# Optimization experiments

Measured on AMD Instinct MI355X. Metric: run time of the kernel, lower is better.

Reference implementation:

```python
import jax, jax.numpy as jnp
import numpy as np
from jax import lax

# dims
B, T_MEL, N_MEL, L_TXT, D_TXT = 8, 400, 80, 128, 512
E, HID, EMB, N_SPK = 256, 256, 128, 100
H = HID // 2  # per-direction LSTM hidden


def setup_inputs() -> dict:
    key = jax.random.key(0)
    ks = jax.random.split(key, 16)
    def n(k, shape, s=0.02):
        return jax.random.normal(k, shape, jnp.float32) * s
    return {
        "x": n(ks[0], (B, N_MEL, T_MEL), 1.0),
        "input_lengths": jax.random.randint(ks[1], (B,), T_MEL // 2, T_MEL + 1).astype(jnp.int32),
        "text": n(ks[2], (B, L_TXT, D_TXT), 1.0),
        "text_lengths": jax.random.randint(ks[3], (B,), L_TXT // 2, L_TXT + 1).astype(jnp.int32),
        "Wx": n(ks[4], (E, N_MEL)), "bx": jnp.zeros((E,), jnp.float32),
        "Wq": n(ks[5], (E, D_TXT)), "bq": jnp.zeros((E,), jnp.float32),
        "Wout": n(ks[6], (E, E)), "bout": jnp.zeros((E,), jnp.float32),
        "v": jax.random.normal(ks[7], (E, 1), jnp.float32) * 0.1,
        "lstm_wih": n(ks[8], (2, 2, 4 * H, HID)),
        "lstm_whh": n(ks[9], (2, 2, 4 * H, H)),
        "lstm_bih": jnp.zeros((2, 2, 4 * H), jnp.float32),
        "lstm_bhh": jnp.zeros((2, 2, 4 * H), jnp.float32),
        "p1_w": n(ks[10], (EMB, HID)), "p1_b": jnp.zeros((EMB,), jnp.float32),
        "p2_w": n(ks[11], (N_SPK, EMB)), "p2_b": jnp.zeros((N_SPK,), jnp.float32),
    }


def _run_lstm(x, Wih, Whh, bih, bhh):
    # x: [B, L, in] -> outputs [B, L, H]; PyTorch gate order i,f,g,o
    h0 = jnp.zeros((x.shape[0], Whh.shape[1]), x.dtype)
    c0 = jnp.zeros_like(h0)
    def step(carry, xt):
        h, c = carry
        g = xt @ Wih.T + h @ Whh.T + (bih + bhh)
        i, f, gg, o = jnp.split(g, 4, axis=-1)
        c = jax.nn.sigmoid(f) * c + jax.nn.sigmoid(i) * jnp.tanh(gg)
        h = jax.nn.sigmoid(o) * jnp.tanh(c)
        return (h, c), h
    _, hs = lax.scan(step, (h0, c0), x.swapaxes(0, 1))  # scan over time
    return hs.swapaxes(0, 1)


def _reverse_by_length(x, lengths):
    # reverse the first lengths[b] steps of each sequence (pack_padded semantics)
    L = x.shape[1]
    idx = jnp.clip(lengths[:, None] - 1 - jnp.arange(L)[None, :], 0, L - 1)
    return jnp.take_along_axis(x, idx[:, :, None], axis=1)


def reference(x, input_lengths, text, text_lengths, Wx, bx, Wq, bq, Wout, bout, v,
              lstm_wih, lstm_whh, lstm_bih, lstm_bhh, p1_w, p1_b, p2_w, p2_b):
    # ---- vectorized VanillaAttention over all text tokens ----
    mels = x.swapaxes(1, 2)                       # [B, T, M]
    x1 = mels @ Wx.T + bx                         # [B, T, E]   linear_x
    q1 = text @ Wq.T + bq                         # [B, L, E]   linear_q
    # v^T @ out_linear(tanh(.)) == tanh(.) @ (Wout^T v) + v . bout
    w = Wout.T @ v[:, 0]                          # [E]
    c = bout @ v[:, 0]                            # scalar
    s = jnp.tanh(x1[:, None, :, :] + q1[:, :, None, :])   # [B, L, T, E]
    scores = jnp.einsum('blte,e->blt', s, w) + c           # [B, L, T]
    mel_mask = jnp.arange(T_MEL)[None, :] < input_lengths[:, None]   # [B, T]
    scores = jnp.where(mel_mask[:, None, :], scores, -jnp.inf)
    scores = jax.nn.softmax(scores, axis=-1)
    contexts = jnp.einsum('blt,bte->ble', scores, x1)       # [B, L, E]
    h = q1 + contexts                                       # LSTM input

    # ---- 2-layer bidirectional LSTM (packed semantics via per-length reversal) ----
    for layer in range(2):
        fwd = _run_lstm(h, lstm_wih[layer, 0], lstm_whh[layer, 0], lstm_bih[layer, 0], lstm_bhh[layer, 0])
        rev = _reverse_by_length(h, text_lengths)
        bwd = _run_lstm(rev, lstm_wih[layer, 1], lstm_whh[layer, 1], lstm_bih[layer, 1], lstm_bhh[layer, 1])
        bwd = _reverse_by_length(bwd, text_lengths)
        h = jnp.concatenate([fwd, bwd], axis=-1)            # [B, L, HID]

    # ---- masked mean pool (pad_packed zeros the padding before the sum) ----
    txt_mask = (jnp.arange(L_TXT)[None, :] < text_lengths[:, None]).astype(h.dtype)
    pooled = (h * txt_mask[:, :, None]).sum(axis=1) / text_lengths[:, None].astype(h.dtype)

    out = jnp.tanh(pooled @ p1_w.T + p1_b)
    embeddings = out / jnp.linalg.norm(out, axis=1, keepdims=True)
    logits = out @ p2_w.T + p2_b
    return logits, embeddings, scores
```

## Files before the change

### kernel.cpp

```cpp
#include <hip/hip_runtime.h>
#include <hip/hip_bf16.h>
#include <math.h>

#define B 8
#define T_MEL 400
#define N_MEL 80
#define L_TXT 128
#define D_TXT 512
#define E 256
#define HID 256
#define EMB 128
#define N_SPK 100
#define HH 128

#define OFF_W      0
#define OFF_C      256
#define OFF_WXT    272
#define OFF_WQT    (OFF_WXT + N_MEL*E)
#define OFF_WIHT   (OFF_WQT + D_TXT*E)
#define OFF_BSUM   (OFF_WIHT + 2*2*256*512)
#define OFF_X1     (OFF_BSUM + 2048)
#define OFF_Q1     (OFF_X1 + B*T_MEL*E)
#define OFF_G      OFF_X1
#define OFF_H0     (OFF_Q1 + B*L_TXT*E)
#define OFF_O1     (OFF_H0 + B*L_TXT*E)
#define OFF_HS0    OFF_H0
#define OFF_POOL   OFF_O1
#define OFF_WG     (OFF_O1 + 4096)

typedef _Float16 half2v __attribute__((ext_vector_type(2)));

__device__ __forceinline__ float fast_sigmoid(float x){ return 1.f/(1.f+__expf(-x)); }
__device__ __forceinline__ float fast_tanh(float x){ float e=__expf(2.f*x); return 1.f - 2.f/(e+1.f); }

__device__ __forceinline__ float fdot2(uint a, uint b, float c){
  half2v ha = __builtin_bit_cast(half2v, a);
  half2v hb = __builtin_bit_cast(half2v, b);
#if __has_builtin(__builtin_amdgcn_fdot2)
  return __builtin_amdgcn_fdot2(ha, hb, c, false);
#else
  float r;
  asm("v_dot2_f32_f16 %0, %1, %2, %3" : "=v"(r) : "v"(a), "v"(b), "v"(c));
  return r;
#endif
}
__device__ __forceinline__ uint packh2(float a, float b){
  union { _Float16 h[2]; uint u; } x;
  x.h[0] = (_Float16)a; x.h[1] = (_Float16)b; return x.u;
}

__global__ __launch_bounds__(256) void k_prep(const float* __restrict__ Wout, const float* __restrict__ bout,
                       const float* __restrict__ v,    const float* __restrict__ Wx,
                       const float* __restrict__ Wq,   const float* __restrict__ wih,
                       const float* __restrict__ bih,  const float* __restrict__ bhh,
                       const float* __restrict__ whh,  float* __restrict__ ws){
  __shared__ __align__(16) float tile[64][81];
  __shared__ __align__(16) uint  utile[64][129];
  int blk = blockIdx.x, tid = threadIdx.x;
  if (blk == 0){
    float acc = 0.f;
    for (int j=0;j<E;j++) acc += Wout[j*E + tid] * v[j];
    ws[OFF_W + tid] = acc;
    if (tid==0){ float c=0.f; for(int j=0;j<E;j++) c += bout[j]*v[j]; ws[OFF_C]=c; }
  } else if (blk <= 4){
    int e0 = (blk-1)*64;
    for (int idx = tid; idx < 64*20; idx += 256){
      int e = idx/20, c4 = idx%20;
      float4 vv = *(const float4*)&Wx[(size_t)(e0+e)*N_MEL + 4*c4];
      tile[e][4*c4]=vv.x; tile[e][4*c4+1]=vv.y; tile[e][4*c4+2]=vv.z; tile[e][4*c4+3]=vv.w;
    }
    __syncthreads();
    for (int idx = tid; idx < N_MEL*64; idx += 256){
      int m = idx>>6, e = idx&63;
      ws[OFF_WXT + m*E + e0 + e] = tile[e][m];
    }
  } else if (blk <= 36){
    int t = blk-5; int e0 = (t&3)*64, k0 = (t>>2)*64;
    for (int idx = tid; idx < 64*16; idx += 256){
      int e = idx>>4, c = idx&15;
      float4 vv = *(const float4*)&Wq[(size_t)(e0+e)*D_TXT + k0 + 4*c];
      tile[e][4*c]=vv.x; tile[e][4*c+1]=vv.y; tile[e][4*c+2]=vv.z; tile[e][4*c+3]=vv.w;
    }
    __syncthreads();
    for (int idx = tid; idx < 64*64; idx += 256){
      int k = idx>>6, e = idx&63;
      ws[OFF_WQT + (k0+k)*E + e0 + e] = tile[e][k];
    }
  } else if (blk <= 68){
    int t = blk-37; int ld = t>>3, g0 = (t&7)*64;
    for (int idx = tid; idx < 64*64; idx += 256){
      int g = idx>>6, c = idx&63;
      float4 vv = *(const float4*)&wih[((size_t)(ld*512+g0+g))*256 + 4*c];
      utile[g][2*c]   = packh2(vv.x, vv.y);
      utile[g][2*c+1] = packh2(vv.z, vv.w);
    }
    __syncthreads();
    uint* wout = (uint*)(ws + OFF_WIHT) + (size_t)ld*128*512;
    for (int idx = tid; idx < 128*64; idx += 256){
      int k2 = idx>>6, g = idx&63;
      wout[(size_t)k2*512 + g0 + g] = utile[g][k2];
    }
  } else if (blk == 69){
    for (int i = tid; i < 2048; i += 256)
      ws[OFF_BSUM + i] = bih[i] + bhh[i];
  } else {
    int bp = blk - 70;
    int ld = bp >> 2, w = bp & 3;
    uint* wg = (uint*)(ws + OFF_WG) + ((size_t)ld*4 + w)*8192;
    for (int ii = 0; ii < 32; ii++){
      int i = ii*256 + tid;
      int r  = i >> 11;
      int jj = (i >> 8) & 7;
      int l  = (i >> 2) & 63;
      int k  = i & 3;
      int u  = w*32 + (l >> 1);
      int hf = l & 1;
      const float* src = whh + ((size_t)(ld*512 + r*128 + u))*HH + 64*hf + jj*8 + 2*k;
      wg[i] = packh2(src[0], src[1]);
    }
  }
}

__global__ __launch_bounds__(256) void k_xq(const float* __restrict__ x,    const float* __restrict__ bx,
                                            const float* __restrict__ text, const float* __restrict__ bq,
                                            float* __restrict__ ws){
  __shared__ float sbuf[2048];
  int blk = blockIdx.x, tid = threadIdx.x;
  if (blk < 800){
    int b = blk/100; int t0 = (blk%100)*4;
    float (*sx)[4] = (float(*)[4])sbuf;
    for (int i = tid; i < N_MEL*4; i += 256){
      int m = i>>2, ii = i&3;
      sx[m][ii] = x[(b*N_MEL+m)*T_MEL + t0 + ii];
    }
    __syncthreads();
    float bxe = bx[tid];
    float a0=bxe,a1=bxe,a2=bxe,a3=bxe;
    const float* wxt = ws + OFF_WXT;
    #pragma unroll 4
    for (int m=0;m<N_MEL;m++){
      float w = wxt[m*E + tid];
      a0 += sx[m][0]*w; a1 += sx[m][1]*w; a2 += sx[m][2]*w; a3 += sx[m][3]*w;
    }
    float* x1 = ws + OFF_X1 + (b*T_MEL + t0)*E + tid;
    x1[0]=a0; x1[E]=a1; x1[2*E]=a2; x1[3*E]=a3;
  } else {
    int bb = blk - 800;
    int b = bb/32; int l0 = (bb%32)*4;
    float (*st)[D_TXT] = (float(*)[D_TXT])sbuf;
    for (int i = tid; i < 4*D_TXT; i += 256){
      int li = i / D_TXT, k = i % D_TXT;
      st[li][k] = text[(b*L_TXT + l0 + li)*D_TXT + k];
    }
    __syncthreads();
    float bqe = bq[tid];
    float a0=bqe,a1=bqe,a2=bqe,a3=bqe;
    const float* wqt = ws + OFF_WQT;
    #pragma unroll 2
    for (int k=0;k<D_TXT;k++){
      float w = wqt[k*E + tid];
      a0 += st[0][k]*w; a1 += st[1][k]*w; a2 += st[2][k]*w; a3 += st[3][k]*w;
    }
    float* q1 = ws + OFF_Q1 + (b*L_TXT + l0)*E + tid;
    q1[0]=a0; q1[E]=a1; q1[2*E]=a2; q1[3*E]=a3;
  }
}

__global__ __launch_bounds__(256) void k_score(const int* __restrict__ mel_len,
                                               float* __restrict__ ws,
                                               float* __restrict__ d_out){
  int blk = blockIdx.x; int b = blk >> 7; int l = blk & 127;
  int tid = threadIdx.x; int lane = tid & 63; int wv = tid >> 6;
  __shared__ __align__(16) float sl[T_MEL];
  __shared__ float red[8];
  const float* x1 = ws + OFF_X1 + b*T_MEL*E;
  const float* q1 = ws + OFF_Q1 + (b*L_TXT+l)*E;
  int g = lane >> 4, i = lane & 15;
  float qv[16], wvv[16];
  {
    const float4* q4 = (const float4*)(q1 + i*16);
    const float4* w4 = (const float4*)(ws + OFF_W + i*16);
    #pragma unroll
    for (int j=0;j<4;j++){
      float4 a = q4[j]; qv[4*j]=a.x; qv[4*j+1]=a.y; qv[4*j+2]=a.z; qv[4*j+3]=a.w;
      float4 c = w4[j]; wvv[4*j]=c.x; wvv[4*j+1]=c.y; wvv[4*j+2]=c.z; wvv[4*j+3]=c.w;
    }
  }
  float cc = ws[OFF_C];
  int len = mel_len[b];
  #pragma unroll 2
  for (int iter=0; iter<25; iter++){
    int t = iter*16 + wv*4 + g;
    const float4* xr = (const float4*)(x1 + t*E + i*16);
    float s = 0.f;
    #pragma unroll
    for (int j=0;j<4;j++){
      float4 xv = xr[j];
      s += wvv[4*j+0]*fast_tanh(xv.x + qv[4*j+0]);
      s += wvv[4*j+1]*fast_tanh(xv.y + qv[4*j+1]);
      s += wvv[4*j+2]*fast_tanh(xv.z + qv[4*j+2]);
      s += wvv[4*j+3]*fast_tanh(xv.w + qv[4*j+3]);
    }
    s += __shfl_xor(s,1); s += __shfl_xor(s,2);
    s += __shfl_xor(s,4); s += __shfl_xor(s,8);
    if (i==0) sl[t] = s + cc;
  }
  __syncthreads();
  float mx = -3.0e38f;
  for (int t = tid; t < T_MEL; t += 256) if (t < len) mx = fmaxf(mx, sl[t]);
  #pragma unroll
  for (int off=32; off>=1; off>>=1) mx = fmaxf(mx, __shfl_xor(mx, off));
  if (lane==0) red[wv] = mx;
  __syncthreads();
  mx = fmaxf(fmaxf(red[0],red[1]),fmaxf(red[2],red[3]));
  float se = 0.f;
  for (int t = tid; t < T_MEL; t += 256){
    float p = (t < len) ? __expf(sl[t]-mx) : 0.f;
    sl[t] = p; se += p;
  }
  #pragma unroll
  for (int off=32; off>=1; off>>=1) se += __shfl_xor(se, off);
  if (lane==0) red[4+wv] = se;
  __syncthreads();
  float rsum = 1.f/(red[4]+red[5]+red[6]+red[7]);
  float* sc_out = d_out + 1824 + (b*L_TXT + l)*T_MEL;
  for (int t = tid; t < T_MEL; t += 256){
    float p = sl[t]*rsum;
    sl[t] = p; sc_out[t] = p;
  }
  __syncthreads();
  float a = 0.f;
  int e = tid;
  for (int t = 0; t < T_MEL; t += 4){
    float4 p4 = *(const float4*)&sl[t];
    a += p4.x*x1[(t  )*E+e] + p4.y*x1[(t+1)*E+e]
       + p4.z*x1[(t+2)*E+e] + p4.w*x1[(t+3)*E+e];
  }
  ws[OFF_H0 + (b*L_TXT+l)*E + e] = q1[e] + a;
}

__global__ __launch_bounds__(512) void k_gates(const float* __restrict__ in,
                                               const float* __restrict__ hs,
                                               const int* __restrict__ txt_len,
                                               float* __restrict__ gates, int layer,
                                               float* __restrict__ ws){
  int idx = blockIdx.x; int tt = idx & 15; int dir = (idx>>4)&1; int b = idx>>5;
  int tid = threadIdx.x;
  __shared__ __align__(16) uint sih[8][128];
  __shared__ float outb[8][512];
  int len = txt_len[b];
  for (int i = tid; i < 8*128; i += 512){
    int r = i >> 7, k2 = i & 127;
    int t = tt*8 + r;
    int row = dir ? max(0, len-1-t) : t;
    float va, vb;
    if (layer == 0){
      const float2 p = *(const float2*)&in[((size_t)(b*L_TXT + row))*HID + 2*k2];
      va = p.x; vb = p.y;
    } else {
      int k = 2*k2; int d = k >> 7, u = k & 127;
      int sidx = (d==0) ? row : (row < len ? len-1-row : 0);
      const float2 p = *(const float2*)&hs[(((size_t)d*L_TXT + sidx)*8 + b)*128 + u];
      va = p.x; vb = p.y;
    }
    sih[r][k2] = packh2(va, vb);
  }
  __syncthreads();
  int ld = layer*2 + dir;
  int g = tid;
  float bsum = ws[OFF_BSUM + ld*512 + g];
  float acc[8];
  #pragma unroll
  for (int r=0;r<8;r++) acc[r] = bsum;
  const uint* wt2 = (const uint*)(ws + OFF_WIHT) + (size_t)ld*128*512 + g;
  for (int k4=0; k4<128; k4+=4){
    uint w0 = wt2[(k4  )*512];
    uint w1 = wt2[(k4+1)*512];
    uint w2 = wt2[(k4+2)*512];
    uint w3 = wt2[(k4+3)*512];
    #pragma unroll
    for (int r=0;r<8;r++){
      uint4 s4 = *(const uint4*)&sih[r][k4];
      acc[r] = fdot2(s4.x, w0, acc[r]);
      acc[r] = fdot2(s4.y, w1, acc[r]);
      acc[r] = fdot2(s4.z, w2, acc[r]);
      acc[r] = fdot2(s4.w, w3, acc[r]);
    }
  }
  #pragma unroll
  for (int r=0;r<8;r++) outb[r][g] = acc[r];
  __syncthreads();
  float* go = gates + (((size_t)(dir*L_TXT + tt*8)*8) + b)*512;
  int src = (tid & 3)*128 + (tid >> 2);
  #pragma unroll
  for (int r=0;r<8;r++) go[(size_t)r*8*512 + tid] = outb[r][src];
}

__global__ __launch_bounds__(256) void k_scan(const float* __restrict__ Gp,
                                              const uint* __restrict__ wg,
                                              const int* __restrict__ txt_len,
                                              float* __restrict__ hseq,
                                              float* __restrict__ pooled, int layer){
  __shared__ uint wlds[22528];
  int dir = blockIdx.x & 1; int b = blockIdx.x >> 1;
  int tid = threadIdx.x;
  int l = tid & 63, w = tid >> 6;
  int u  = tid >> 1;
  int hf = tid & 1;

  const uint* wgp = wg + (((size_t)(layer*2+dir))*4 + w)*8192 + l*4;
  uint4 wi[8], wf[8], wgg[8], wo[8];
  #pragma unroll
  for (int jj=0;jj<8;jj++){
    wi [jj] = *(const uint4*)(wgp + (jj   )*256);
    wf [jj] = *(const uint4*)(wgp + ( 8+jj)*256);
    wgg[jj] = *(const uint4*)(wgp + (16+jj)*256);
    wo [jj] = *(const uint4*)(wgp + (24+jj)*256);
  }
  #pragma unroll
  for (int jj=0;jj<8;jj++){
    asm volatile("" : "+v"(wi [jj].x), "+v"(wi [jj].y), "+v"(wi [jj].z), "+v"(wi [jj].w));
    asm volatile("" : "+v"(wf [jj].x), "+v"(wf [jj].y), "+v"(wf [jj].z), "+v"(wf [jj].w));
    asm volatile("" : "+v"(wgg[jj].x), "+v"(wgg[jj].y), "+v"(wgg[jj].z), "+v"(wgg[jj].w));
    asm volatile("" : "+v"(wo [jj].x), "+v"(wo [jj].y), "+v"(wo [jj].z), "+v"(wo [jj].w));
  }

  if (tid < 128) wlds[tid] = 0;
  int len = txt_len[b];
  bool pool = (layer == 1);

  const float* gb = Gp + ((size_t)(dir*L_TXT)*8 + b)*512 + u*4;
  float4 q = *(const float4*)gb;
  float c_reg = 0.f, psum = 0.f;
  __syncthreads();

  for (int s=0; s<L_TXT; s++){
    const float* gn = gb + (size_t)(s+1 < L_TXT ? s+1 : s)*4096;
    float4 qn = *(const float4*)gn;
    const uint4* hp = (const uint4*)(wlds + (s&1)*64 + hf*32);
    float a0 = hf ? 0.f : q.x;
    float a1 = hf ? 0.f : q.y;
    float a2 = hf ? 0.f : q.z;
    float a3 = hf ? 0.f : q.w;
    #pragma unroll
    for (int jj=0;jj<8;jj++){
      uint4 hv = hp[jj];
      uint4 w0 = wi [jj];
      uint4 w1 = wf [jj];
      uint4 w2 = wgg[jj];
      uint4 w3 = wo [jj];
      a0 = fdot2(w0.x,hv.x,a0); a0 = fdot2(w0.y,hv.y,a0);
      a0 = fdot2(w0.z,hv.z,a0); a0 = fdot2(w0.w,hv.w,a0);
      a1 = fdot2(w1.x,hv.x,a1); a1 = fdot2(w1.y,hv.y,a1);
      a1 = fdot2(w1.z,hv.z,a1); a1 = fdot2(w1.w,hv.w,a1);
      a2 = fdot2(w2.x,hv.x,a2); a2 = fdot2(w2.y,hv.y,a2);
      a2 = fdot2(w2.z,hv.z,a2); a2 = fdot2(w2.w,hv.w,a2);
      a3 = fdot2(w3.x,hv.x,a3); a3 = fdot2(w3.y,hv.y,a3);
      a3 = fdot2(w3.z,hv.z,a3); a3 = fdot2(w3.w,hv.w,a3);
    }
    a0 += __shfl_xor(a0, 1);
    a1 += __shfl_xor(a1, 1);
    a2 += __shfl_xor(a2, 1);
    a3 += __shfl_xor(a3, 1);
    float i_ = fast_sigmoid(a0);
    float f_ = fast_sigmoid(a1);
    float g_ = fast_tanh   (a2);
    float o_ = fast_sigmoid(a3);
    c_reg = f_*c_reg + i_*g_;
    float h = o_*fast_tanh(c_reg);
    float hn = __shfl_xor(h, 2);
    if (hf==0 && !(u&1)) wlds[((s+1)&1)*64 + (u>>1)] = packh2(h, hn);
    if (pool){
      if (s < len) psum += h;
    } else {
      if (hf==0) hseq[(((size_t)dir*L_TXT + s)*8 + b)*128 + u] = h;
    }
    q = qn;
    __syncthreads();
  }
  if (pool && hf==0) pooled[((size_t)(dir*8+b))*128 + u] = psum;
}

__global__ __launch_bounds__(256) void k_final(const float* __restrict__ pooled,
                                               const int* __restrict__ txt_len,
                                               const float* __restrict__ p1w,
                                               const float* __restrict__ p1b,
                                               const float* __restrict__ p2w,
                                               const float* __restrict__ p2b,
                                               float* __restrict__ d_out){
  int b = blockIdx.x; int tid = threadIdx.x;
  __shared__ float pl[HID];
  __shared__ float ol[EMB];
  __shared__ float nrm;
  int len = txt_len[b];
  int d = tid >> 7, u = tid & 127;
  pl[tid] = pooled[((size_t)(d*8+b))*128 + u] / (float)len;
  __syncthreads();
  if (tid < EMB){
    float a = p1b[tid];
    for (int k=0;k<HID;k++) a += pl[k]*p1w[tid*HID+k];
    ol[tid] = fast_tanh(a);
  }
  __syncthreads();
  if (tid == 0){
    float q = 0.f;
    for (int k=0;k<EMB;k++) q += ol[k]*ol[k];
    nrm = rsqrtf(q);
  }
  __syncthreads();
  if (tid < EMB) d_out[800 + b*EMB + tid] = ol[tid]*nrm;
  if (tid < N_SPK){
    float a = p2b[tid];
    for (int k=0;k<EMB;k++) a += ol[k]*p2w[tid*EMB+k];
    d_out[b*N_SPK + tid] = a;
  }
}

extern "C" void kernel_launch(void* const* d_in, const int* in_sizes, int n_in,
                              void* d_out, int out_size, void* d_ws, size_t ws_size,
                              hipStream_t stream) {
  const float* x       = (const float*)d_in[0];
  const int*   mel_len = (const int*)  d_in[1];
  const float* text    = (const float*)d_in[2];
  const int*   txt_len = (const int*)  d_in[3];
  const float* Wx      = (const float*)d_in[4];
  const float* bx      = (const float*)d_in[5];
  const float* Wq      = (const float*)d_in[6];
  const float* bq      = (const float*)d_in[7];
  const float* Wout    = (const float*)d_in[8];
  const float* bout    = (const float*)d_in[9];
  const float* v       = (const float*)d_in[10];
  const float* wih     = (const float*)d_in[11];
  const float* whh     = (const float*)d_in[12];
  const float* bih     = (const float*)d_in[13];
  const float* bhh     = (const float*)d_in[14];
  const float* p1w     = (const float*)d_in[15];
  const float* p1b     = (const float*)d_in[16];
  const float* p2w     = (const float*)d_in[17];
  const float* p2b     = (const float*)d_in[18];
  float* ws  = (float*)d_ws;
  float* out = (float*)d_out;
  const uint* wg = (const uint*)(ws + OFF_WG);

  k_prep <<<86, 256, 0, stream>>>(Wout, bout, v, Wx, Wq, wih, bih, bhh, whh, ws);
  k_xq   <<<1056, 256, 0, stream>>>(x, bx, text, bq, ws);
  k_score<<<1024, 256, 0, stream>>>(mel_len, ws, out);

  float* G = ws + OFF_G;
  k_gates<<<256, 512, 0, stream>>>(ws + OFF_H0, ws + OFF_HS0, txt_len, G, 0, ws);
  k_scan <<<16, 256, 0, stream>>>(G, wg, txt_len, ws + OFF_HS0, ws + OFF_POOL, 0);
  k_gates<<<256, 512, 0, stream>>>(ws + OFF_H0, ws + OFF_HS0, txt_len, G, 1, ws);
  k_scan <<<16, 256, 0, stream>>>(G, wg, txt_len, ws + OFF_HS0, ws + OFF_POOL, 1);

  k_final<<<8, 256, 0, stream>>>(ws + OFF_POOL, txt_len, p1w, p1b, p2w, p2b, out);
}
```

Measured before the change: 384.3 us.

## Split LSTM scan gates across twice as many threads per block

```diff
diff --git a/kernel.cpp b/kernel.cpp
--- a/kernel.cpp
+++ b/kernel.cpp
@@ -105,17 +105,19 @@
       ws[OFF_BSUM + i] = bih[i] + bhh[i];
   } else {
     int bp = blk - 70;
-    int ld = bp >> 2, w = bp & 3;
-    uint* wg = (uint*)(ws + OFF_WG) + ((size_t)ld*4 + w)*8192;
-    for (int ii = 0; ii < 32; ii++){
+    int ld = bp >> 3, w = bp & 7;
+    uint* wg = (uint*)(ws + OFF_WG) + ((size_t)ld*8 + w)*4096;
+    for (int ii = 0; ii < 16; ii++){
       int i = ii*256 + tid;
-      int r  = i >> 11;
-      int jj = (i >> 8) & 7;
+      int j  = i >> 8;
       int l  = (i >> 2) & 63;
       int k  = i & 3;
-      int u  = w*32 + (l >> 1);
+      int rsel = j >> 3, jj = j & 7;
+      int u  = w*16 + (l >> 2);
+      int pr = (l >> 1) & 1;
       int hf = l & 1;
-      const float* src = whh + ((size_t)(ld*512 + r*128 + u))*HH + 64*hf + jj*8 + 2*k;
+      int row = rsel ? (256 + pr*128 + u) : (pr*128 + u);
+      const float* src = whh + ((size_t)(ld*512 + row))*HH + 64*hf + jj*8 + 2*k;
       wg[i] = packh2(src[0], src[1]);
     }
   }
@@ -296,7 +298,7 @@
   for (int r=0;r<8;r++) go[(size_t)r*8*512 + tid] = outb[r][src];
 }
 
-__global__ __launch_bounds__(256) void k_scan(const float* __restrict__ Gp,
+__global__ __launch_bounds__(512) void k_scan(const float* __restrict__ Gp,
                                               const uint* __restrict__ wg,
                                               const int* __restrict__ txt_len,
                                               float* __restrict__ hseq,
@@ -305,24 +307,21 @@
   int dir = blockIdx.x & 1; int b = blockIdx.x >> 1;
   int tid = threadIdx.x;
   int l = tid & 63, w = tid >> 6;
-  int u  = tid >> 1;
+  int u  = tid >> 2;
+  int pr = (tid >> 1) & 1;
   int hf = tid & 1;
 
-  const uint* wgp = wg + (((size_t)(layer*2+dir))*4 + w)*8192 + l*4;
-  uint4 wi[8], wf[8], wgg[8], wo[8];
+  const uint* wgp = wg + (((size_t)(layer*2+dir))*8 + w)*4096 + l*4;
+  uint4 wA[8], wB[8];
   #pragma unroll
   for (int jj=0;jj<8;jj++){
-    wi [jj] = *(const uint4*)(wgp + (jj   )*256);
-    wf [jj] = *(const uint4*)(wgp + ( 8+jj)*256);
-    wgg[jj] = *(const uint4*)(wgp + (16+jj)*256);
-    wo [jj] = *(const uint4*)(wgp + (24+jj)*256);
+    wA[jj] = *(const uint4*)(wgp + (jj   )*256);
+    wB[jj] = *(const uint4*)(wgp + (8+jj)*256);
   }
   #pragma unroll
   for (int jj=0;jj<8;jj++){
-    asm volatile("" : "+v"(wi [jj].x), "+v"(wi [jj].y), "+v"(wi [jj].z), "+v"(wi [jj].w));
-    asm volatile("" : "+v"(wf [jj].x), "+v"(wf [jj].y), "+v"(wf [jj].z), "+v"(wf [jj].w));
-    asm volatile("" : "+v"(wgg[jj].x), "+v"(wgg[jj].y), "+v"(wgg[jj].z), "+v"(wgg[jj].w));
-    asm volatile("" : "+v"(wo [jj].x), "+v"(wo [jj].y), "+v"(wo [jj].z), "+v"(wo [jj].w));
+    asm volatile("" : "+v"(wA[jj].x), "+v"(wA[jj].y), "+v"(wA[jj].z), "+v"(wA[jj].w));
+    asm volatile("" : "+v"(wB[jj].x), "+v"(wB[jj].y), "+v"(wB[jj].z), "+v"(wB[jj].w));
   }
 
   if (tid < 128) wlds[tid] = 0;
@@ -330,55 +329,49 @@
   bool pool = (layer == 1);
 
   const float* gb = Gp + ((size_t)(dir*L_TXT)*8 + b)*512 + u*4;
-  float4 q = *(const float4*)gb;
+  float gA = gb[pr], gB = gb[pr+2];
   float c_reg = 0.f, psum = 0.f;
   __syncthreads();
 
   for (int s=0; s<L_TXT; s++){
     const float* gn = gb + (size_t)(s+1 < L_TXT ? s+1 : s)*4096;
-    float4 qn = *(const float4*)gn;
+    float nA = gn[pr], nB = gn[pr+2];
     const uint4* hp = (const uint4*)(wlds + (s&1)*64 + hf*32);
-    float a0 = hf ? 0.f : q.x;
-    float a1 = hf ? 0.f : q.y;
-    float a2 = hf ? 0.f : q.z;
-    float a3 = hf ? 0.f : q.w;
+    float aA = hf ? 0.f : gA;
+    float aB = hf ? 0.f : gB;
     #pragma unroll
     for (int jj=0;jj<8;jj++){
       uint4 hv = hp[jj];
-      uint4 w0 = wi [jj];
-      uint4 w1 = wf [jj];
-      uint4 w2 = wgg[jj];
-      uint4 w3 = wo [jj];
-      a0 = fdot2(w0.x,hv.x,a0); a0 = fdot2(w0.y,hv.y,a0);
-      a0 = fdot2(w0.z,hv.z,a0); a0 = fdot2(w0.w,hv.w,a0);
-      a1 = fdot2(w1.x,hv.x,a1); a1 = fdot2(w1.y,hv.y,a1);
-      a1 = fdot2(w1.z,hv.z,a1); a1 = fdot2(w1.w,hv.w,a1);
-      a2 = fdot2(w2.x,hv.x,a2); a2 = fdot2(w2.y,hv.y,a2);
-      a2 = fdot2(w2.z,hv.z,a2); a2 = fdot2(w2.w,hv.w,a2);
-      a3 = fdot2(w3.x,hv.x,a3); a3 = fdot2(w3.y,hv.y,a3);
-      a3 = fdot2(w3.z,hv.z,a3); a3 = fdot2(w3.w,hv.w,a3);
-    }
-    a0 += __shfl_xor(a0, 1);
-    a1 += __shfl_xor(a1, 1);
-    a2 += __shfl_xor(a2, 1);
-    a3 += __shfl_xor(a3, 1);
-    float i_ = fast_sigmoid(a0);
-    float f_ = fast_sigmoid(a1);
-    float g_ = fast_tanh   (a2);
-    float o_ = fast_sigmoid(a3);
-    c_reg = f_*c_reg + i_*g_;
-    float h = o_*fast_tanh(c_reg);
-    float hn = __shfl_xor(h, 2);
-    if (hf==0 && !(u&1)) wlds[((s+1)&1)*64 + (u>>1)] = packh2(h, hn);
+      uint4 a = wA[jj];
+      uint4 c = wB[jj];
+      aA = fdot2(a.x,hv.x,aA); aA = fdot2(a.y,hv.y,aA);
+      aA = fdot2(a.z,hv.z,aA); aA = fdot2(a.w,hv.w,aA);
+      aB = fdot2(c.x,hv.x,aB); aB = fdot2(c.y,hv.y,aB);
+      aB = fdot2(c.z,hv.z,aB); aB = fdot2(c.w,hv.w,aB);
+    }
+    aA += __shfl_xor(aA, 1);
+    aB += __shfl_xor(aB, 1);
+    float vA = fast_sigmoid(aA);
+    float vB = pr ? fast_sigmoid(aB) : fast_tanh(aB);
+    float xA = __shfl_xor(vA, 2);
+    float xB = __shfl_xor(vB, 2);
+    float iv = pr ? xA : vA;
+    float fv = pr ? vA : xA;
+    float gv = pr ? xB : vB;
+    float ov = pr ? vB : xB;
+    c_reg = fv*c_reg + iv*gv;
+    float h = ov*fast_tanh(c_reg);
+    float hn = __shfl_xor(h, 4);
+    if (hf==0 && pr==0 && !(u&1)) wlds[((s+1)&1)*64 + (u>>1)] = packh2(h, hn);
     if (pool){
       if (s < len) psum += h;
     } else {
-      if (hf==0) hseq[(((size_t)dir*L_TXT + s)*8 + b)*128 + u] = h;
-    }
-    q = qn;
-    __syncthreads();
-  }
-  if (pool && hf==0) pooled[((size_t)(dir*8+b))*128 + u] = psum;
+      if (hf==0 && pr==0) hseq[(((size_t)dir*L_TXT + s)*8 + b)*128 + u] = h;
+    }
+    gA = nA; gB = nB;
+    __syncthreads();
+  }
+  if (pool && hf==0 && pr==0) pooled[((size_t)(dir*8+b))*128 + u] = psum;
 }
 
 __global__ __launch_bounds__(256) void k_final(const float* __restrict__ pooled,
@@ -442,15 +435,15 @@
   float* out = (float*)d_out;
   const uint* wg = (const uint*)(ws + OFF_WG);
 
-  k_prep <<<86, 256, 0, stream>>>(Wout, bout, v, Wx, Wq, wih, bih, bhh, whh, ws);
+  k_prep <<<102, 256, 0, stream>>>(Wout, bout, v, Wx, Wq, wih, bih, bhh, whh, ws);
   k_xq   <<<1056, 256, 0, stream>>>(x, bx, text, bq, ws);
   k_score<<<1024, 256, 0, stream>>>(mel_len, ws, out);
 
   float* G = ws + OFF_G;
   k_gates<<<256, 512, 0, stream>>>(ws + OFF_H0, ws + OFF_HS0, txt_len, G, 0, ws);
-  k_scan <<<16, 256, 0, stream>>>(G, wg, txt_len, ws + OFF_HS0, ws + OFF_POOL, 0);
+  k_scan <<<16, 512, 0, stream>>>(G, wg, txt_len, ws + OFF_HS0, ws + OFF_POOL, 0);
   k_gates<<<256, 512, 0, stream>>>(ws + OFF_H0, ws + OFF_HS0, txt_len, G, 1, ws);
-  k_scan <<<16, 256, 0, stream>>>(G, wg, txt_len, ws + OFF_HS0, ws + OFF_POOL, 1);
+  k_scan <<<16, 512, 0, stream>>>(G, wg, txt_len, ws + OFF_HS0, ws + OFF_POOL, 1);
 
   k_final<<<8, 256, 0, stream>>>(ws + OFF_POOL, txt_len, p1w, p1b, p2w, p2b, out);
 }
```

Result: slower. 404.3 us (+5.2%).
